# Optimization experiments

Hardware: AMD Instinct MI355X
Metric: run time of the kernel (lower is better)

## Reference

```python
import jax, jax.numpy as jnp
import numpy as np

L, D, H, P = 4096, 512, 512, 16  # seq_len, feature_dim, attention_hidden_dim, padding_size


def setup_inputs() -> dict:
    key = jax.random.key(0)
    k1, k2, k3, k4 = jax.random.split(key, 4)
    x = jax.random.normal(k1, (L, D), dtype=jnp.float32)
    s = 1.0 / np.sqrt(D).astype(np.float32)
    Ww = jax.random.uniform(k2, (H, D), jnp.float32, -s, s)   # nn.Linear(D, H, bias=False).weight
    Wu = jax.random.uniform(k3, (H, D), jnp.float32, -s, s)
    sv = 1.0 / np.sqrt(H).astype(np.float32)
    Wv = jax.random.uniform(k4, (1, H), jnp.float32, -sv, sv)  # nn.Linear(H, 1, bias=False).weight
    return {"x": x, "Ww": Ww, "Wu": Wu, "Wv": Wv}


def _window_gather(x):
    # zero-pad P rows on each end of the sequence, then for each position i
    # gather the 2P neighbors (P left, P right), excluding the center.
    xp = jnp.pad(x, ((P, P), (0, 0)))
    off = jnp.concatenate([jnp.arange(P), jnp.arange(P + 1, 2 * P + 1)])  # [2P]
    idx = jnp.arange(x.shape[0])[:, None] + off[None, :]                  # [L, 2P]
    return xp[idx]                                                        # [L, 2P, D]


def reference(x, Ww, Wu, Wv):
    x_local = _window_gather(x)                                  # [L, 2P, D]
    wx = x @ Ww.T                                                # [L, H] (center, computed once vs torch repeat)
    ux = jnp.einsum('lwd,hd->lwh', x_local, Wu)                  # [L, 2P, H]
    energy = jnp.tanh(wx[:, None, :] + ux)                       # [L, 2P, H]
    scores = jnp.einsum('lwh,h->lw', energy, Wv[0])              # [L, 2P]
    attn = jax.nn.softmax(scores, axis=1)                        # softmax over window
    g = jnp.einsum('lw,lwd->ld', attn, x_local)                  # [L, D]
    return g
```

## Files before the change

kernel.cpp:

```cpp
#include <hip/hip_runtime.h>

#define L_SEQ 4096
#define D_DIM 512
#define H_DIM 512
#define P_PAD 16
#define LB 4
#define NR (LB + 2 * P_PAD)
#define LOG2E2 2.885390081777927f
#define LOG2E  1.4426950408889634f

typedef __bf16 bf16x8 __attribute__((ext_vector_type(8)));
typedef float  f32x4  __attribute__((ext_vector_type(4)));
typedef unsigned short u16x8 __attribute__((ext_vector_type(8)));

extern "C" __device__ float __ocml_native_exp2_f32(float);

__device__ __forceinline__ float exp2_fast(float x) {
#if __has_builtin(__builtin_amdgcn_exp2f)
    return __builtin_amdgcn_exp2f(x);
#else
    return __ocml_native_exp2_f32(x);
#endif
}

__device__ __forceinline__ ushort f2bf(float f) {
    unsigned u = __float_as_uint(f);
    return (ushort)((u + 0x7FFFu + ((u >> 16) & 1u)) >> 16);
}
__device__ __forceinline__ float bf2f(ushort s) {
    return __uint_as_float((unsigned)s << 16);
}

__device__ __forceinline__ float readlane_f(float v, int sl) {
    return __uint_as_float(__builtin_amdgcn_readlane(__float_as_uint(v), sl));
}

__global__ __launch_bounds__(256, 2) void dual_gemm_mfma(
    const float* __restrict__ x, const float* __restrict__ Ww,
    const float* __restrict__ Wu, ushort* __restrict__ Ewb, ushort* __restrict__ Eub)
{
    const float* Bw = blockIdx.z ? Wu : Ww;
    ushort*      out = blockIdx.z ? Eub : Ewb;
    const int m0 = blockIdx.x * 128;
    const int n0 = blockIdx.y * 64;

    __shared__ __align__(16) ushort As[2][128 * 64];
    __shared__ __align__(16) ushort Bs[2][64 * 64];

    const int tid  = threadIdx.x;
    const int wv   = tid >> 6;
    const int lane = tid & 63;
    const int wm   = (wv >> 1) * 64;
    const int wn   = (wv & 1) * 32;
    const int lr   = lane & 15;
    const int lg   = lane >> 4;
    const int rx   = lr & 7;

    f32x4 acc[4][2] = {};

    auto stage = [&](int t, int buf) {
        const int k0 = t * 64;
        #pragma unroll
        for (int i = 0; i < 4; ++i) {
            int c = i * 256 + tid, row = c >> 3, q = c & 7;
            const float* s = x + (size_t)(m0 + row) * D_DIM + k0 + q * 8;
            float4 f0 = *(const float4*)s;
            float4 f1 = *(const float4*)(s + 4);
            u16x8 hv;
            hv[0] = f2bf(f0.x); hv[1] = f2bf(f0.y); hv[2] = f2bf(f0.z); hv[3] = f2bf(f0.w);
            hv[4] = f2bf(f1.x); hv[5] = f2bf(f1.y); hv[6] = f2bf(f1.z); hv[7] = f2bf(f1.w);
            *(u16x8*)&As[buf][row * 64 + ((q ^ (row & 7)) * 8)] = hv;
        }
        #pragma unroll
        for (int i = 0; i < 2; ++i) {
            int c = i * 256 + tid, row = c >> 3, q = c & 7;
            const float* s = Bw + (size_t)(n0 + row) * D_DIM + k0 + q * 8;
            float4 f0 = *(const float4*)s;
            float4 f1 = *(const float4*)(s + 4);
            u16x8 hv;
            hv[0] = f2bf(f0.x); hv[1] = f2bf(f0.y); hv[2] = f2bf(f0.z); hv[3] = f2bf(f0.w);
            hv[4] = f2bf(f1.x); hv[5] = f2bf(f1.y); hv[6] = f2bf(f1.z); hv[7] = f2bf(f1.w);
            *(u16x8*)&Bs[buf][row * 64 + ((q ^ (row & 7)) * 8)] = hv;
        }
    };

    auto compute = [&](int buf) {
        #pragma unroll
        for (int kk = 0; kk < 2; ++kk) {
            bf16x8 a[4], b[2];
            #pragma unroll
            for (int mi = 0; mi < 4; ++mi)
                a[mi] = *(const bf16x8*)&As[buf][(wm + mi * 16 + lr) * 64 +
                                                 (((kk * 4 + lg) ^ rx) * 8)];
            #pragma unroll
            for (int ni = 0; ni < 2; ++ni)
                b[ni] = *(const bf16x8*)&Bs[buf][(wn + ni * 16 + lr) * 64 +
                                                 (((kk * 4 + lg) ^ rx) * 8)];
            #pragma unroll
            for (int mi = 0; mi < 4; ++mi)
                #pragma unroll
                for (int ni = 0; ni < 2; ++ni)
                    acc[mi][ni] = __builtin_amdgcn_mfma_f32_16x16x32_bf16(
                        a[mi], b[ni], acc[mi][ni], 0, 0, 0);
        }
    };

    stage(0, 0);
    __syncthreads();
    #pragma unroll
    for (int t = 0; t < 7; ++t) {
        stage(t + 1, (t + 1) & 1);
        compute(t & 1);
        __syncthreads();
    }
    compute(1);

    #pragma unroll
    for (int mi = 0; mi < 4; ++mi)
        #pragma unroll
        for (int ni = 0; ni < 2; ++ni)
            #pragma unroll
            for (int r = 0; r < 4; ++r)
                out[(size_t)(m0 + wm + mi * 16 + lg * 4 + r) * H_DIM + n0 + wn + ni * 16 + lr] =
                    f2bf(exp2_fast(LOG2E2 * acc[mi][ni][r]));
}

template<bool EDGE>
__device__ __forceinline__ void fused_body(
    const ushort* __restrict__ Ewb, const ushort* __restrict__ Eub,
    const float* __restrict__ Wv, const float* __restrict__ x,
    float* __restrict__ g, int l0,
    float sc_lds[LB][32], float at_lds[LB][32])
{
    const int tid  = threadIdx.x;
    const int wv   = tid >> 6;
    const int lane = tid & 63;
    const int li   = wv >> 1;
    const int half = wv & 1;
    const int l    = l0 + li;
    const int col  = tid;

    float ewr[8], wvn[8];
    {
        u16x8 ew8 = *(const u16x8*)&Ewb[(size_t)l * H_DIM + lane * 8];
        const f32x4* wvp = (const f32x4*)&Wv[lane * 8];
        f32x4 v0 = wvp[0], v1 = wvp[1];
        #pragma unroll
        for (int e = 0; e < 8; ++e) ewr[e] = bf2f(ew8[e]);
        #pragma unroll
        for (int e = 0; e < 4; ++e) { wvn[e] = -2.0f * v0[e]; wvn[e + 4] = -2.0f * v1[e]; }
    }

    float aoob = 0.0f;
    if (EDGE && (l < P_PAD || l >= L_SEQ - P_PAD)) {
        #pragma unroll
        for (int e = 0; e < 8; ++e)
            aoob = __builtin_fmaf(wvn[e], __builtin_amdgcn_rcpf(ewr[e] + 1.0f), aoob);
    }

    const ushort* base = Eub + (size_t)l * H_DIM + lane * 8;
    #pragma unroll
    for (int q = 0; q < 4; ++q) {
        u16x8 u[4];
        int valid[4];
        #pragma unroll
        for (int wi = 0; wi < 4; ++wi) {
            const int w = half * 16 + q * 4 + wi;
            const int j = (w < P_PAD) ? (w - P_PAD) : (w - P_PAD + 1);
            if (EDGE) {
                int n = l + j;
                valid[wi] = ((unsigned)n < (unsigned)L_SEQ);
                n = min(max(n, 0), L_SEQ - 1);
                u[wi] = *(const u16x8*)&Eub[(size_t)n * H_DIM + lane * 8];
            } else {
                u[wi] = *(const u16x8*)(base + j * H_DIM);
            }
        }
        float a4[4];
        #pragma unroll
        for (int wi = 0; wi < 4; ++wi) {
            float a = 0.0f;
            #pragma unroll
            for (int e = 0; e < 8; ++e) {
                float eu = bf2f(u[wi][e]);
                float qq = __builtin_fmaf(ewr[e], eu, 1.0f);
                a = __builtin_fmaf(wvn[e], __builtin_amdgcn_rcpf(qq), a);
            }
            if (EDGE) a = valid[wi] ? a : aoob;
            a4[wi] = a;
        }
        const bool b0 = lane & 1, b1 = lane & 2;
        float s01 = b0 ? a4[0] : a4[1];
        float r01 = __shfl_xor(s01, 1);
        float c0  = (b0 ? a4[1] : a4[0]) + r01;
        float s23 = b0 ? a4[2] : a4[3];
        float r23 = __shfl_xor(s23, 1);
        float c1  = (b0 ? a4[3] : a4[2]) + r23;
        float s2  = b1 ? c0 : c1;
        float r2  = __shfl_xor(s2, 2);
        float c   = (b1 ? c1 : c0) + r2;
        c += __shfl_xor(c, 4);
        c += __shfl_xor(c, 8);
        c += __shfl_xor(c, 16);
        c += __shfl_xor(c, 32);
        if (lane < 4) sc_lds[li][half * 16 + q * 4 + lane] = c;
    }

    float xv[NR];
    #pragma unroll
    for (int t = 0; t < NR; ++t) {
        int n = l0 - P_PAD + t;
        if (EDGE) n = min(max(n, 0), L_SEQ - 1);
        xv[t] = x[(size_t)n * D_DIM + col];
    }
    __syncthreads();

    if (tid < LB * 32) {
        const int ll = tid >> 5, w = tid & 31;
        float s0 = sc_lds[ll][w];
        float m = s0;
        #pragma unroll
        for (int off = 16; off; off >>= 1) m = fmaxf(m, __shfl_xor(m, off, 32));
        float e = exp2_fast((s0 - m) * LOG2E);
        float sum = e;
        #pragma unroll
        for (int off = 16; off; off >>= 1) sum += __shfl_xor(sum, off, 32);
        at_lds[ll][w] = e * __builtin_amdgcn_rcpf(sum);
    }
    __syncthreads();

    float2 aw2 = ((const float2*)at_lds)[lane];

    #pragma unroll
    for (int li2 = 0; li2 < LB; ++li2) {
        float a = 0.0f;
        #pragma unroll
        for (int w = 0; w < 32; ++w) {
            const int j = (w < P_PAD) ? (w - P_PAD) : (w - P_PAD + 1);
            const int t = j + P_PAD + li2;
            const int k = li2 * 32 + w;
            float aw = readlane_f((k & 1) ? aw2.y : aw2.x, k >> 1);
            if (EDGE) {
                const int n = l0 + li2 + j;
                if (n < 0 || n >= L_SEQ) aw = 0.0f;
            }
            a = __builtin_fmaf(aw, xv[t], a);
        }
        g[(size_t)(l0 + li2) * D_DIM + col] = a;
    }
}

__global__ __launch_bounds__(512, 4) void scores_gather_kernel(
    const ushort* __restrict__ Ewb, const ushort* __restrict__ Eub,
    const float* __restrict__ Wv, const float* __restrict__ x,
    float* __restrict__ g)
{
    const int bid = (blockIdx.x & 7) * 128 + (blockIdx.x >> 3);
    const int l0  = bid * LB;

    __shared__ __align__(16) float sc_lds[LB][32];
    __shared__ __align__(16) float at_lds[LB][32];

    if (l0 >= P_PAD && l0 + LB + P_PAD <= L_SEQ)
        fused_body<false>(Ewb, Eub, Wv, x, g, l0, sc_lds, at_lds);
    else
        fused_body<true>(Ewb, Eub, Wv, x, g, l0, sc_lds, at_lds);
}

extern "C" void kernel_launch(void* const* d_in, const int* in_sizes, int n_in,
                              void* d_out, int out_size, void* d_ws, size_t ws_size,
                              hipStream_t stream) {
    const float* x  = (const float*)d_in[0];
    const float* Ww = (const float*)d_in[1];
    const float* Wu = (const float*)d_in[2];
    const float* Wv = (const float*)d_in[3];
    float* g = (float*)d_out;

    ushort* Ewb = (ushort*)d_ws;
    ushort* Eub = Ewb + (size_t)L_SEQ * H_DIM;

    dual_gemm_mfma<<<dim3(L_SEQ / 128, H_DIM / 64, 2), 256, 0, stream>>>(x, Ww, Wu, Ewb, Eub);
    scores_gather_kernel<<<dim3(L_SEQ / LB), 512, 0, stream>>>(Ewb, Eub, Wv, x, g);
}
```

Before: 37.93 us.

## Compute both weight GEMMs in one block sharing the staged x tile

Each block of the dual GEMM now loads and converts the x tile once and multiplies it against both Ww and Wu, keeping two accumulator sets. The grid loses its z dimension, so there are half as many blocks. This removes the duplicated global reads and bf16 conversion of x. In exchange, accumulator registers double, LDS use grows, and fewer blocks are available to fill the GPU, which may hurt occupancy under the 2-blocks-per-SM launch bound.

```diff
diff --git a/kernel.cpp b/kernel.cpp
--- a/kernel.cpp
+++ b/kernel.cpp
@@ -39,13 +39,11 @@
     const float* __restrict__ x, const float* __restrict__ Ww,
     const float* __restrict__ Wu, ushort* __restrict__ Ewb, ushort* __restrict__ Eub)
 {
-    const float* Bw = blockIdx.z ? Wu : Ww;
-    ushort*      out = blockIdx.z ? Eub : Ewb;
     const int m0 = blockIdx.x * 128;
     const int n0 = blockIdx.y * 64;
 
     __shared__ __align__(16) ushort As[2][128 * 64];
-    __shared__ __align__(16) ushort Bs[2][64 * 64];
+    __shared__ __align__(16) ushort Bs[2][2][64 * 64];
 
     const int tid  = threadIdx.x;
     const int wv   = tid >> 6;
@@ -56,52 +54,57 @@
     const int lg   = lane >> 4;
     const int rx   = lr & 7;
 
-    f32x4 acc[4][2] = {};
+    f32x4 acc[2][4][2] = {};
+
+    auto cvt8 = [&](const float* s) {
+        float4 f0 = *(const float4*)s;
+        float4 f1 = *(const float4*)(s + 4);
+        u16x8 hv;
+        hv[0] = f2bf(f0.x); hv[1] = f2bf(f0.y); hv[2] = f2bf(f0.z); hv[3] = f2bf(f0.w);
+        hv[4] = f2bf(f1.x); hv[5] = f2bf(f1.y); hv[6] = f2bf(f1.z); hv[7] = f2bf(f1.w);
+        return hv;
+    };
 
     auto stage = [&](int t, int buf) {
         const int k0 = t * 64;
         #pragma unroll
         for (int i = 0; i < 4; ++i) {
             int c = i * 256 + tid, row = c >> 3, q = c & 7;
-            const float* s = x + (size_t)(m0 + row) * D_DIM + k0 + q * 8;
-            float4 f0 = *(const float4*)s;
-            float4 f1 = *(const float4*)(s + 4);
-            u16x8 hv;
-            hv[0] = f2bf(f0.x); hv[1] = f2bf(f0.y); hv[2] = f2bf(f0.z); hv[3] = f2bf(f0.w);
-            hv[4] = f2bf(f1.x); hv[5] = f2bf(f1.y); hv[6] = f2bf(f1.z); hv[7] = f2bf(f1.w);
-            *(u16x8*)&As[buf][row * 64 + ((q ^ (row & 7)) * 8)] = hv;
+            *(u16x8*)&As[buf][row * 64 + ((q ^ (row & 7)) * 8)] =
+                cvt8(x + (size_t)(m0 + row) * D_DIM + k0 + q * 8);
         }
         #pragma unroll
         for (int i = 0; i < 2; ++i) {
             int c = i * 256 + tid, row = c >> 3, q = c & 7;
-            const float* s = Bw + (size_t)(n0 + row) * D_DIM + k0 + q * 8;
-            float4 f0 = *(const float4*)s;
-            float4 f1 = *(const float4*)(s + 4);
-            u16x8 hv;
-            hv[0] = f2bf(f0.x); hv[1] = f2bf(f0.y); hv[2] = f2bf(f0.z); hv[3] = f2bf(f0.w);
-            hv[4] = f2bf(f1.x); hv[5] = f2bf(f1.y); hv[6] = f2bf(f1.z); hv[7] = f2bf(f1.w);
-            *(u16x8*)&Bs[buf][row * 64 + ((q ^ (row & 7)) * 8)] = hv;
+            *(u16x8*)&Bs[buf][0][row * 64 + ((q ^ (row & 7)) * 8)] =
+                cvt8(Ww + (size_t)(n0 + row) * D_DIM + k0 + q * 8);
+            *(u16x8*)&Bs[buf][1][row * 64 + ((q ^ (row & 7)) * 8)] =
+                cvt8(Wu + (size_t)(n0 + row) * D_DIM + k0 + q * 8);
         }
     };
 
     auto compute = [&](int buf) {
         #pragma unroll
         for (int kk = 0; kk < 2; ++kk) {
-            bf16x8 a[4], b[2];
+            bf16x8 a[4], b[2][2];
             #pragma unroll
             for (int mi = 0; mi < 4; ++mi)
                 a[mi] = *(const bf16x8*)&As[buf][(wm + mi * 16 + lr) * 64 +
                                                  (((kk * 4 + lg) ^ rx) * 8)];
             #pragma unroll
-            for (int ni = 0; ni < 2; ++ni)
-                b[ni] = *(const bf16x8*)&Bs[buf][(wn + ni * 16 + lr) * 64 +
-                                                 (((kk * 4 + lg) ^ rx) * 8)];
-            #pragma unroll
-            for (int mi = 0; mi < 4; ++mi)
+            for (int wgt = 0; wgt < 2; ++wgt)
                 #pragma unroll
                 for (int ni = 0; ni < 2; ++ni)
-                    acc[mi][ni] = __builtin_amdgcn_mfma_f32_16x16x32_bf16(
-                        a[mi], b[ni], acc[mi][ni], 0, 0, 0);
+                    b[wgt][ni] = *(const bf16x8*)&Bs[buf][wgt][(wn + ni * 16 + lr) * 64 +
+                                                              (((kk * 4 + lg) ^ rx) * 8)];
+            #pragma unroll
+            for (int wgt = 0; wgt < 2; ++wgt)
+                #pragma unroll
+                for (int mi = 0; mi < 4; ++mi)
+                    #pragma unroll
+                    for (int ni = 0; ni < 2; ++ni)
+                        acc[wgt][mi][ni] = __builtin_amdgcn_mfma_f32_16x16x32_bf16(
+                            a[mi], b[wgt][ni], acc[wgt][mi][ni], 0, 0, 0);
         }
     };
 
@@ -116,13 +119,17 @@
     compute(1);
 
     #pragma unroll
-    for (int mi = 0; mi < 4; ++mi)
-        #pragma unroll
-        for (int ni = 0; ni < 2; ++ni)
-            #pragma unroll
-            for (int r = 0; r < 4; ++r)
-                out[(size_t)(m0 + wm + mi * 16 + lg * 4 + r) * H_DIM + n0 + wn + ni * 16 + lr] =
-                    f2bf(exp2_fast(LOG2E2 * acc[mi][ni][r]));
+    for (int wgt = 0; wgt < 2; ++wgt) {
+        ushort* out = wgt ? Eub : Ewb;
+        #pragma unroll
+        for (int mi = 0; mi < 4; ++mi)
+            #pragma unroll
+            for (int ni = 0; ni < 2; ++ni)
+                #pragma unroll
+                for (int r = 0; r < 4; ++r)
+                    out[(size_t)(m0 + wm + mi * 16 + lg * 4 + r) * H_DIM + n0 + wn + ni * 16 + lr] =
+                        f2bf(exp2_fast(LOG2E2 * acc[wgt][mi][ni][r]));
+    }
 }
 
 template<bool EDGE>
@@ -279,6 +286,6 @@
     ushort* Ewb = (ushort*)d_ws;
     ushort* Eub = Ewb + (size_t)L_SEQ * H_DIM;
 
-    dual_gemm_mfma<<<dim3(L_SEQ / 128, H_DIM / 64, 2), 256, 0, stream>>>(x, Ww, Wu, Ewb, Eub);
+    dual_gemm_mfma<<<dim3(L_SEQ / 128, H_DIM / 64), 256, 0, stream>>>(x, Ww, Wu, Ewb, Eub);
     scores_gather_kernel<<<dim3(L_SEQ / LB), 512, 0, stream>>>(Ewb, Eub, Wv, x, g);
 }
```

Measured after the change: 40.11 us. 1.06x slower.
